# Kernel optimization log

Measured on AMD Instinct MI355X. Metric: run time of the kernel, lower is better.

The kernel has to match this reference:

```python
import jax, jax.numpy as jnp
import numpy as np

N_NODES = 100000
N_EDGES = 1200000
MAX_ATOM_TYPE = 100
NUM_FEATURES = 92
GC_DIM = 64          # pre_layer_dim == gc_dim == CGConv channels
NUM_RBF = 32
NUM_GC_LAYERS = 4
CUTOFF_UPPER = 5.0
BN_EPS = 1e-5


def setup_inputs() -> dict:
    key = jax.random.key(0)
    ks = jax.random.split(key, 12)
    atom_types = jax.random.randint(ks[0], (N_NODES,), 0, MAX_ATOM_TYPE, dtype=jnp.int32)
    pos = jax.random.uniform(ks[1], (N_NODES, 3), dtype=jnp.float32) * 6.0  # box side 6 -> many dists < cutoff
    edge_index = jax.random.randint(ks[2], (2, N_EDGES), 0, N_NODES, dtype=jnp.int32)
    # parameters
    emb = jax.random.normal(ks[3], (MAX_ATOM_TYPE, NUM_FEATURES), dtype=jnp.float32)
    s = 1.0 / np.sqrt(NUM_FEATURES)
    pre_W = jax.random.uniform(ks[4], (NUM_FEATURES, GC_DIM), minval=-s, maxval=s, dtype=jnp.float32)
    pre_b = jnp.zeros((GC_DIM,), jnp.float32)
    zdim = 2 * GC_DIM + NUM_RBF  # [x_i, x_j, edge_attr]
    sz = 1.0 / np.sqrt(zdim)
    Wf = jax.random.uniform(ks[5], (NUM_GC_LAYERS, zdim, GC_DIM), minval=-sz, maxval=sz, dtype=jnp.float32)
    bf = jnp.zeros((NUM_GC_LAYERS, GC_DIM), jnp.float32)
    Ws = jax.random.uniform(ks[6], (NUM_GC_LAYERS, zdim, GC_DIM), minval=-sz, maxval=sz, dtype=jnp.float32)
    bs = jnp.zeros((NUM_GC_LAYERS, GC_DIM), jnp.float32)
    bn_gamma = jnp.ones((NUM_GC_LAYERS, GC_DIM), jnp.float32)
    bn_beta = jnp.zeros((NUM_GC_LAYERS, GC_DIM), jnp.float32)
    # ExpNormalSmearing (torchmd-net) init
    start = np.exp(-CUTOFF_UPPER)
    means = jnp.asarray(np.linspace(start, 1.0, NUM_RBF), jnp.float32)
    betas = jnp.full((NUM_RBF,), (2.0 / NUM_RBF * (1.0 - start)) ** -2, jnp.float32)
    return {"atom_types": atom_types, "pos": pos, "edge_index": edge_index,
            "emb": emb, "pre_W": pre_W, "pre_b": pre_b,
            "Wf": Wf, "bf": bf, "Ws": Ws, "bs": bs,
            "bn_gamma": bn_gamma, "bn_beta": bn_beta,
            "means": means, "betas": betas}


def _forward(atom_types, pos, edge_index, emb, pre_W, pre_b, Wf, bf, Ws, bs,
             bn_gamma, bn_beta, means, betas):
    src, dst = edge_index[0], edge_index[1]
    # distance (edge_vec = pos[src] - pos[dst])
    vec = pos[src] - pos[dst]                                  # [E,3]
    dist = jnp.sqrt(jnp.sum(vec * vec, axis=-1) + 1e-12)       # [E]
    # expnorm RBF with cosine cutoff (cutoff_lower = 0)
    cutoff = 0.5 * (jnp.cos(dist * (np.pi / CUTOFF_UPPER)) + 1.0) * (dist < CUTOFF_UPPER)
    alpha = 5.0 / CUTOFF_UPPER
    edge_attr = cutoff[:, None] * jnp.exp(
        -betas * (jnp.exp(-alpha * dist)[:, None] - means) ** 2)  # [E,NUM_RBF]
    # embedding + pre layer
    x = emb[atom_types]                                        # [N,F]
    x = jax.nn.relu(x @ pre_W + pre_b)                         # [N,C]
    # mean-aggregation degree (scatter-mean denominator)
    deg = jax.ops.segment_sum(jnp.ones_like(dist), dst, num_segments=N_NODES)
    inv_deg = jnp.where(deg > 0, 1.0 / jnp.maximum(deg, 1.0), 0.0)[:, None]
    for l in range(NUM_GC_LAYERS):
        # CGConv: z = [x_i, x_j, e]; out = x + mean_j(sigmoid(lin_f(z)) * softplus(lin_s(z)))
        z = jnp.concatenate([x[dst], x[src], edge_attr], axis=-1)   # [E, 2C+R]
        msg = jax.nn.sigmoid(z @ Wf[l] + bf[l]) * jax.nn.softplus(z @ Ws[l] + bs[l])
        agg = jax.ops.segment_sum(msg, dst, num_segments=N_NODES) * inv_deg
        x = x + agg
        # BatchNorm1d (batch statistics, biased var, as in torch training mode)
        mu = jnp.mean(x, axis=0)
        var = jnp.mean((x - mu) ** 2, axis=0)
        x = (x - mu) * jax.lax.rsqrt(var + BN_EPS) * bn_gamma[l] + bn_beta[l]
    return x


def reference(atom_types, pos, edge_index, emb, pre_W, pre_b, Wf, bf, Ws, bs,
              bn_gamma, bn_beta, means, betas):
    return _forward(atom_types, pos, edge_index, emb, pre_W, pre_b, Wf, bf, Ws, bs,
                    bn_gamma, bn_beta, means, betas)
```

## Files before the change

### kernel.cpp

```cpp
#include <hip/hip_runtime.h>
#include <math.h>

#define N_NODES 100000
#define N_EDGES 1200000
#define GC 64
#define RBF 32
#define NLAYERS 4
#define NF 92
#define NATOM 100
#define BN_EPS 1e-5f
#define TILE_GRID 2048
#define NWIN (N_EDGES / 16)
#define LOG2E 1.44269504f
#define LN2 0.69314718f

typedef _Float16 half8 __attribute__((ext_vector_type(8)));
typedef _Float16 half4 __attribute__((ext_vector_type(4)));
typedef _Float16 half2v __attribute__((ext_vector_type(2)));
typedef float f32x4 __attribute__((ext_vector_type(4)));
union U32H2 { unsigned int u; half2v h; };

__global__ __launch_bounds__(256) void deg_kernel(
    const int* __restrict__ ei, int* __restrict__ deg)
{
    int e = blockIdx.x * 256 + threadIdx.x;
    if (e >= N_EDGES) return;
    atomicAdd(&deg[ei[N_EDGES + e]], 1);
}

__global__ __launch_bounds__(256) void scan_a_kernel(const int* __restrict__ deg, int* __restrict__ bsums)
{
    __shared__ int sm[256];
    int tid = threadIdx.x;
    int i = blockIdx.x * 256 + tid;
    int v = (i < N_NODES) ? deg[i] : 0;
    sm[tid] = v;
    __syncthreads();
    for (int s = 128; s > 0; s >>= 1) {
        if (tid < s) sm[tid] += sm[tid + s];
        __syncthreads();
    }
    if (tid == 0) bsums[blockIdx.x] = sm[0];
}

__global__ __launch_bounds__(512) void scan_b_kernel(const int* __restrict__ bsums, int* __restrict__ boffs)
{
    __shared__ int sm[512];
    int tid = threadIdx.x;
    int v = (tid < 391) ? bsums[tid] : 0;
    sm[tid] = v;
    __syncthreads();
    for (int off = 1; off < 512; off <<= 1) {
        int t = (tid >= off) ? sm[tid - off] : 0;
        __syncthreads();
        sm[tid] += t;
        __syncthreads();
    }
    boffs[tid] = (tid == 0) ? 0 : sm[tid - 1];
}

__global__ __launch_bounds__(256) void scan_c_kernel(
    const int* __restrict__ deg, const int* __restrict__ boffs,
    int* __restrict__ row_st, float* __restrict__ inv_deg)
{
    __shared__ int sm[256];
    int tid = threadIdx.x;
    int i = blockIdx.x * 256 + tid;
    int v = (i < N_NODES) ? deg[i] : 0;
    sm[tid] = v;
    __syncthreads();
    for (int off = 1; off < 256; off <<= 1) {
        int t = (tid >= off) ? sm[tid - off] : 0;
        __syncthreads();
        sm[tid] += t;
        __syncthreads();
    }
    if (i <= N_NODES) row_st[i] = boffs[blockIdx.x] + sm[tid] - v;
    if (i < N_NODES) inv_deg[i] = (v > 0) ? (1.0f / (float)v) : 0.0f;
}

__global__ __launch_bounds__(256) void scatter_perm_kernel(
    const int* __restrict__ ei, const int* __restrict__ row_st,
    int* __restrict__ cursor, int2* __restrict__ csr_sd)
{
    int e = blockIdx.x * 256 + threadIdx.x;
    if (e >= N_EDGES) return;
    int s = ei[e];
    int d = ei[N_EDGES + e];
    int p = atomicAdd(&cursor[d], 1);
    csr_sd[row_st[d] + p] = make_int2(s, d);
}

__global__ __launch_bounds__(256) void split_kernel(
    const int2* __restrict__ csr_sd, int* __restrict__ csr_src, int* __restrict__ csr_dst)
{
    int i = blockIdx.x * 256 + threadIdx.x;
    if (i >= N_EDGES) return;
    int2 v = csr_sd[i];
    csr_src[i] = v.x;
    csr_dst[i] = v.y;
}

__global__ __launch_bounds__(256) void rbf_kernel(
    const int* __restrict__ csr_src, const int* __restrict__ csr_dst,
    const float* __restrict__ pos,
    const float* __restrict__ means, const float* __restrict__ betas,
    unsigned int* __restrict__ ea)
{
    int idx = blockIdx.x * 256 + threadIdx.x;
    if (idx >= N_EDGES) return;
    int s = csr_src[idx];
    int d = csr_dst[idx];
    float dx = pos[s * 3 + 0] - pos[d * 3 + 0];
    float dy = pos[s * 3 + 1] - pos[d * 3 + 1];
    float dz = pos[s * 3 + 2] - pos[d * 3 + 2];
    float dist = sqrtf(dx * dx + dy * dy + dz * dz + 1e-12f);

    float cut = 0.0f;
    if (dist < 5.0f) cut = 0.5f * (__cosf(dist * 0.6283185307179586f) + 1.0f);
    float ex = __expf(-dist);
    union { _Float16 h[32]; uint4 u[4]; } pk;
#pragma unroll
    for (int k = 0; k < 32; k++) {
        float v = ex - means[k];
        pk.h[k] = (_Float16)(cut * __expf(-betas[k] * v * v));
    }
    uint4* op = (uint4*)(ea + (size_t)idx * 16);
    op[0] = pk.u[0];
    op[1] = pk.u[1];
    op[2] = pk.u[2];
    op[3] = pk.u[3];
}

__global__ __launch_bounds__(256) void window_prep_kernel(
    const int* __restrict__ csr_dst, const float* __restrict__ inv_deg,
    unsigned char* __restrict__ seg8, int* __restrict__ wnode, _Float16* __restrict__ inv_e)
{
    int w = blockIdx.x * 256 + threadIdx.x;
    if (w >= NWIN) return;
    int base = w * 16;
    int prev = -1, s = -1;
    for (int k = 0; k < 16; k++) {
        int d = csr_dst[base + k];
        if (d != prev) { s++; prev = d; wnode[base + s] = d; }
        seg8[base + k] = (unsigned char)s;
        inv_e[base + k] = (_Float16)(inv_deg[d] * LN2);
    }
    for (int m = s + 1; m < 16; m++) wnode[base + m] = -1;
}

__global__ __launch_bounds__(256) void wcvt_kernel(
    const float* __restrict__ Wf, const float* __restrict__ Ws,
    _Float16* __restrict__ wf16, _Float16* __restrict__ ws16)
{
    int i = blockIdx.x * 256 + threadIdx.x;
    int l = i / (160 * GC);
    int r = i - l * 160 * GC;
    int k = r >> 6;
    int col = r & 63;
    size_t o = ((size_t)l * GC + col) * 160 + k;
    wf16[o] = (_Float16)(Wf[i] * LOG2E);
    ws16[o] = (_Float16)(Ws[i] * LOG2E);
}

__global__ __launch_bounds__(64) void atom_table_kernel(
    const float* __restrict__ emb, const float* __restrict__ pre_W,
    const float* __restrict__ pre_b, float* __restrict__ T)
{
    int a = blockIdx.x;
    int c = threadIdx.x;
    float acc = pre_b[c];
    for (int k = 0; k < NF; k++) acc = fmaf(emb[a * NF + k], pre_W[k * GC + c], acc);
    T[a * GC + c] = fmaxf(acc, 0.0f);
}

__global__ __launch_bounds__(256) void xinit_kernel(
    const int* __restrict__ atom_types, const float* __restrict__ T,
    float* __restrict__ x, _Float16* __restrict__ x16)
{
    int i = blockIdx.x * 256 + threadIdx.x;
    int n = i >> 4;
    int a = atom_types[n];
    float4 v = ((const float4*)T)[a * 16 + (i & 15)];
    ((float4*)x)[i] = v;
    half4 h = { (_Float16)v.x, (_Float16)v.y, (_Float16)v.z, (_Float16)v.w };
    ((half4*)x16)[i] = h;
}

static __device__ __forceinline__ void proj_mfma16(
    const _Float16* __restrict__ wf, const _Float16* __restrict__ ws,
    const float* __restrict__ bfv, const float* __restrict__ bsv,
    const half8 Bn[2], int cb, int node, unsigned int* __restrict__ P2u)
{
    const int lane = threadIdx.x & 63;
    const int quad = lane >> 4;
    const int r16 = lane & 15;
    f32x4 accf[2], accs[2];
#pragma unroll
    for (int sub = 0; sub < 2; sub++) {
        accf[sub] = (f32x4){0.f, 0.f, 0.f, 0.f};
        accs[sub] = (f32x4){0.f, 0.f, 0.f, 0.f};
    }
#pragma unroll
    for (int kt = 0; kt < 2; kt++) {
#pragma unroll
        for (int sub = 0; sub < 2; sub++) {
            int chan = cb + sub * 16 + r16;
            half8 a = *(const half8*)(wf + (size_t)chan * 160 + kt * 32 + quad * 8);
            half8 b = *(const half8*)(ws + (size_t)chan * 160 + kt * 32 + quad * 8);
            accf[sub] = __builtin_amdgcn_mfma_f32_16x16x32_f16(a, Bn[kt], accf[sub], 0, 0, 0);
            accs[sub] = __builtin_amdgcn_mfma_f32_16x16x32_f16(b, Bn[kt], accs[sub], 0, 0, 0);
        }
    }
#pragma unroll
    for (int sub = 0; sub < 2; sub++) {
        float4 bf4 = *(const float4*)(bfv + cb + sub * 16 + quad * 4);
        float4 bs4 = *(const float4*)(bsv + cb + sub * 16 + quad * 4);
        half8 h = { (_Float16)(accf[sub][0] + bf4.x * LOG2E), (_Float16)(accs[sub][0] + bs4.x * LOG2E),
                    (_Float16)(accf[sub][1] + bf4.y * LOG2E), (_Float16)(accs[sub][1] + bs4.y * LOG2E),
                    (_Float16)(accf[sub][2] + bf4.z * LOG2E), (_Float16)(accs[sub][2] + bs4.z * LOG2E),
                    (_Float16)(accf[sub][3] + bf4.w * LOG2E), (_Float16)(accs[sub][3] + bs4.w * LOG2E) };
        *(half8*)(P2u + (size_t)node * GC + cb + sub * 16 + quad * 4) = h;
    }
}

__global__ __launch_bounds__(256) void proj_kernel(
    const _Float16* __restrict__ x16,
    const _Float16* __restrict__ wf, const _Float16* __restrict__ ws,
    const float* __restrict__ bfv, const float* __restrict__ bsv,
    unsigned int* __restrict__ P2u)
{
    const int lane = threadIdx.x & 63;
    const int wid = threadIdx.x >> 6;
    const int quad = lane >> 4;
    const int r16 = lane & 15;
    const int wgid = blockIdx.x * 4 + wid;
    const int cb = (wgid & 1) * 32;
    const int nb = (wgid >> 1) * 16;
    half8 Bn[2];
    Bn[0] = *(const half8*)(x16 + (size_t)(nb + r16) * GC + quad * 8);
    Bn[1] = *(const half8*)(x16 + (size_t)(nb + r16) * GC + 32 + quad * 8);
    proj_mfma16(wf, ws, bfv, bsv, Bn, cb, nb + r16, P2u);
}

__global__ __launch_bounds__(256) void bnproj_kernel(
    const float* __restrict__ xn, const float* __restrict__ stats,
    const float* __restrict__ gamma, const float* __restrict__ beta,
    float* __restrict__ xout, _Float16* __restrict__ x16,
    const _Float16* __restrict__ wf, const _Float16* __restrict__ ws,
    const float* __restrict__ bfv, const float* __restrict__ bsv,
    unsigned int* __restrict__ P2u)
{
    __shared__ _Float16 lx[32 * 72];
    const int nb = blockIdx.x * 32;
    const float invN = 1.0f / (float)N_NODES;

#pragma unroll
    for (int rep = 0; rep < 2; rep++) {
        int g = rep * 256 + threadIdx.x;
        int gi = blockIdx.x * 512 + g;
        int node = g >> 4;
        int c4 = (g & 15) * 4;
        float4 v = ((const float4*)xn)[gi];
        float vv[4] = {v.x, v.y, v.z, v.w};
        float o[4];
#pragma unroll
        for (int t = 0; t < 4; t++) {
            int c = c4 + t;
            float mu = stats[c] * invN;
            float var = stats[64 + c] * invN - mu * mu;
            float sc = gamma[c] * rsqrtf(var + BN_EPS);
            o[t] = (vv[t] - mu) * sc + beta[c];
        }
        ((float4*)xout)[gi] = make_float4(o[0], o[1], o[2], o[3]);
        half4 h = { (_Float16)o[0], (_Float16)o[1], (_Float16)o[2], (_Float16)o[3] };
        ((half4*)x16)[gi] = h;
        *(half4*)(lx + node * 72 + c4) = h;
    }
    __syncthreads();

    const int lane = threadIdx.x & 63;
    const int wid = threadIdx.x >> 6;
    const int quad = lane >> 4;
    const int r16 = lane & 15;
    const int cb = (wid & 1) * 32;
    const int tn = (wid >> 1) * 16 + r16;
    half8 Bn[2];
    Bn[0] = *(const half8*)(lx + tn * 72 + quad * 8);
    Bn[1] = *(const half8*)(lx + tn * 72 + 32 + quad * 8);
    proj_mfma16(wf, ws, bfv, bsv, Bn, cb, nb + tn, P2u);
}

static __device__ __forceinline__ void compute_win(
    half8 S0, half8 S1, half8 E, int4 d4, int moff,
    const half8 (&WGF)[3][2], const half8 (&WGS)[3][2],
    int r16, int quad, int cb,
    const unsigned char* __restrict__ seg8, const int* __restrict__ wnode,
    const _Float16* __restrict__ inv_e, const unsigned int* __restrict__ P2u,
    float* __restrict__ x)
{
    unsigned int pv0, pv1, pv2, pv3, pv4, pv5, pv6, pv7;
    {
        const unsigned int* p0 = P2u + (size_t)d4.x * GC + cb + r16;
        const unsigned int* p1 = P2u + (size_t)d4.y * GC + cb + r16;
        const unsigned int* p2 = P2u + (size_t)d4.z * GC + cb + r16;
        const unsigned int* p3 = P2u + (size_t)d4.w * GC + cb + r16;
        pv0 = p0[0];  pv4 = p0[16];
        pv1 = p1[0];  pv5 = p1[16];
        pv2 = p2[0];  pv6 = p2[16];
        pv3 = p3[0];  pv7 = p3[16];
    }
    unsigned int segq = *(const unsigned int*)(seg8 + moff + quad * 4);
    int4 wn4 = *(const int4*)(wnode + moff + quad * 4);
    half4 inv4 = *(const half4*)(inv_e + moff + quad * 4);

    const f32x4 zf = (f32x4){0.0f, 0.0f, 0.0f, 0.0f};
    f32x4 accf[2], accs[2];
    __builtin_amdgcn_s_setprio(1);
#pragma unroll
    for (int ctl = 0; ctl < 2; ctl++) {
        accf[ctl] = __builtin_amdgcn_mfma_f32_16x16x32_f16(S0, WGF[0][ctl], zf, 0, 0, 0);
        accs[ctl] = __builtin_amdgcn_mfma_f32_16x16x32_f16(S0, WGS[0][ctl], zf, 0, 0, 0);
        accf[ctl] = __builtin_amdgcn_mfma_f32_16x16x32_f16(S1, WGF[1][ctl], accf[ctl], 0, 0, 0);
        accs[ctl] = __builtin_amdgcn_mfma_f32_16x16x32_f16(S1, WGS[1][ctl], accs[ctl], 0, 0, 0);
        accf[ctl] = __builtin_amdgcn_mfma_f32_16x16x32_f16(E,  WGF[2][ctl], accf[ctl], 0, 0, 0);
        accs[ctl] = __builtin_amdgcn_mfma_f32_16x16x32_f16(E,  WGS[2][ctl], accs[ctl], 0, 0, 0);
    }
    __builtin_amdgcn_s_setprio(0);

    unsigned int pvv[8] = {pv0, pv1, pv2, pv3, pv4, pv5, pv6, pv7};
    half4 msgh[2];
#pragma unroll
    for (int ctl = 0; ctl < 2; ctl++) {
#pragma unroll
        for (int rr = 0; rr < 4; rr++) {
            U32H2 t; t.u = pvv[ctl * 4 + rr];
            float af = accf[ctl][rr] + (float)t.h.x;
            float as = accs[ctl][rr] + (float)t.h.y;
            float sg = __builtin_amdgcn_rcpf(1.0f + __builtin_amdgcn_exp2f(-af));
            float sp = __builtin_amdgcn_logf(1.0f + __builtin_amdgcn_exp2f(as));
            msgh[ctl][rr] = (_Float16)(sg * sp);
        }
    }
    half4 am;
#pragma unroll
    for (int j = 0; j < 4; j++) {
        int sj = (segq >> (8 * j)) & 0xff;
        am[j] = (sj == r16) ? inv4[j] : (_Float16)0.0f;
    }
    int wa[4] = { wn4.x, wn4.y, wn4.z, wn4.w };
#pragma unroll
    for (int ctl = 0; ctl < 2; ctl++) {
        f32x4 red = __builtin_amdgcn_mfma_f32_16x16x16f16(am, msgh[ctl], zf, 0, 0, 0);
#pragma unroll
        for (int rr = 0; rr < 4; rr++) {
            int nd = wa[rr];
            if (nd >= 0) atomicAdd(&x[(size_t)nd * GC + cb + ctl * 16 + r16], red[rr]);
        }
    }
}

#define LOADSET(S0_, S1_, EE_, SRC_, WW_)                                            \
    S0_ = *(const half8*)(x16 + (size_t)(SRC_) * GC + quad * 8);                     \
    S1_ = *(const half8*)(x16 + (size_t)(SRC_) * GC + 32 + quad * 8);                \
    EE_ = *(const half8*)(ea + ((size_t)(WW_) * 16 + r16) * RBF + quad * 8);

__global__ __launch_bounds__(256, 4) void win_mfma_kernel(
    const _Float16* __restrict__ x16, const _Float16* __restrict__ ea,
    const int* __restrict__ csr_src, const int* __restrict__ csr_dst,
    const unsigned char* __restrict__ seg8, const int* __restrict__ wnode,
    const _Float16* __restrict__ inv_e, const unsigned int* __restrict__ P2u,
    const _Float16* __restrict__ wf16, const _Float16* __restrict__ ws16,
    float* __restrict__ x)
{
    const int lane = threadIdx.x & 63;
    const int wid = __builtin_amdgcn_readfirstlane(threadIdx.x >> 6);
    const int quad = lane >> 4;
    const int r16 = lane & 15;
    const int wgid = blockIdx.x * 4 + wid;
    const int cb = (wgid & 1) * 32;
    int w = wgid >> 1;
    const int NSEQ = TILE_GRID * 2;

    half8 WGF[3][2], WGS[3][2];
#pragma unroll
    for (int ctl = 0; ctl < 2; ctl++) {
        const _Float16* wfp = wf16 + (size_t)(cb + ctl * 16 + r16) * 160 + 64 + quad * 8;
        const _Float16* wsp = ws16 + (size_t)(cb + ctl * 16 + r16) * 160 + 64 + quad * 8;
#pragma unroll
        for (int kt = 0; kt < 3; kt++) {
            WGF[kt][ctl] = *(const half8*)(wfp + kt * 32);
            WGS[kt][ctl] = *(const half8*)(wsp + kt * 32);
        }
    }

    int sA = csr_src[w * 16 + r16];
    int4 d4A = *(const int4*)(csr_dst + w * 16 + quad * 4);
    half8 AS0, AS1, AE;
    LOADSET(AS0, AS1, AE, sA, w);
    int moffA = w * 16;

    int wB = w + NSEQ; if (wB >= NWIN) wB = NWIN - 1;
    int sB = csr_src[wB * 16 + r16];
    int4 d4B = *(const int4*)(csr_dst + wB * 16 + quad * 4);
    half8 BS0, BS1, BE;
    LOADSET(BS0, BS1, BE, sB, wB);
    int moffB = wB * 16;

    int wC = wB + NSEQ; if (wC >= NWIN) wC = NWIN - 1;
    int sC = csr_src[wC * 16 + r16];
    int4 d4C = *(const int4*)(csr_dst + wC * 16 + quad * 4);

    while (true) {
        compute_win(AS0, AS1, AE, d4A, moffA,
                    WGF, WGS, r16, quad, cb, seg8, wnode, inv_e, P2u, x);
        LOADSET(AS0, AS1, AE, sC, wC);
        d4A = d4C; moffA = wC * 16;
        wC += NSEQ; if (wC >= NWIN) wC = NWIN - 1;
        sC = csr_src[wC * 16 + r16];
        d4C = *(const int4*)(csr_dst + wC * 16 + quad * 4);
        w += NSEQ;
        if (w >= NWIN) break;

        compute_win(BS0, BS1, BE, d4B, moffB,
                    WGF, WGS, r16, quad, cb, seg8, wnode, inv_e, P2u, x);
        LOADSET(BS0, BS1, BE, sC, wC);
        d4B = d4C; moffB = wC * 16;
        wC += NSEQ; if (wC >= NWIN) wC = NWIN - 1;
        sC = csr_src[wC * 16 + r16];
        d4C = *(const int4*)(csr_dst + wC * 16 + quad * 4);
        w += NSEQ;
        if (w >= NWIN) break;
    }
}

__global__ __launch_bounds__(256) void stats_kernel(const float* __restrict__ x, float* __restrict__ stats)
{
    const int lane = threadIdx.x & 63;
    const int wid = threadIdx.x >> 6;
    int w = blockIdx.x * 4 + wid;
    float s1 = 0.0f, s2 = 0.0f;
    for (int n = w; n < N_NODES; n += 1024) {
        float v = x[(size_t)n * GC + lane];
        s1 += v;
        s2 = fmaf(v, v, s2);
    }
    __shared__ float rs1[4][64];
    __shared__ float rs2[4][64];
    rs1[wid][lane] = s1;
    rs2[wid][lane] = s2;
    __syncthreads();
    if (threadIdx.x < 64) {
        atomicAdd(&stats[lane], rs1[0][lane] + rs1[1][lane] + rs1[2][lane] + rs1[3][lane]);
    } else if (threadIdx.x < 128) {
        int c = threadIdx.x & 63;
        atomicAdd(&stats[64 + c], rs2[0][c] + rs2[1][c] + rs2[2][c] + rs2[3][c]);
    }
}

__global__ __launch_bounds__(256) void bn_kernel(
    const float* __restrict__ xn, const float* __restrict__ stats,
    const float* __restrict__ gamma, const float* __restrict__ beta,
    float* __restrict__ out)
{
    int i = blockIdx.x * 256 + threadIdx.x;
    int c4 = (i & 15) * 4;
    float4 v = ((const float4*)xn)[i];
    float vv[4] = {v.x, v.y, v.z, v.w};
    float o[4];
    const float invN = 1.0f / (float)N_NODES;
#pragma unroll
    for (int t = 0; t < 4; t++) {
        int c = c4 + t;
        float mu = stats[c] * invN;
        float var = stats[64 + c] * invN - mu * mu;
        float sc = gamma[c] * rsqrtf(var + BN_EPS);
        o[t] = (vv[t] - mu) * sc + beta[c];
    }
    ((float4*)out)[i] = make_float4(o[0], o[1], o[2], o[3]);
}

extern "C" void kernel_launch(void* const* d_in, const int* in_sizes, int n_in,
                              void* d_out, int out_size, void* d_ws, size_t ws_size,
                              hipStream_t stream)
{
    const int* atom_types = (const int*)d_in[0];
    const float* pos = (const float*)d_in[1];
    const int* edge_index = (const int*)d_in[2];
    const float* emb = (const float*)d_in[3];
    const float* pre_W = (const float*)d_in[4];
    const float* pre_b = (const float*)d_in[5];
    const float* Wf = (const float*)d_in[6];
    const float* bf = (const float*)d_in[7];
    const float* Ws = (const float*)d_in[8];
    const float* bs = (const float*)d_in[9];
    const float* gamma = (const float*)d_in[10];
    const float* beta = (const float*)d_in[11];
    const float* means = (const float*)d_in[12];
    const float* betas = (const float*)d_in[13];

    char* base = (char*)d_ws;
    char* p = base;
    auto alloc = [&](size_t bytes) -> char* {
        char* r = p;
        p += (bytes + 255) & ~(size_t)255;
        return r;
    };
    unsigned int* ea = (unsigned int*)alloc((size_t)N_EDGES * RBF * 2);
    float* x = (float*)alloc((size_t)N_NODES * GC * 4);
    _Float16* x16 = (_Float16*)alloc((size_t)N_NODES * GC * 2);
    unsigned int* P2u = (unsigned int*)alloc((size_t)N_NODES * GC * 4);
    int* csr_src = (int*)alloc((size_t)N_EDGES * 4);
    int* csr_dst = (int*)alloc((size_t)N_EDGES * 4);
    int* wnode = (int*)alloc((size_t)N_EDGES * 4);
    unsigned char* seg8 = (unsigned char*)alloc((size_t)N_EDGES);
    _Float16* inv_e = (_Float16*)alloc((size_t)N_EDGES * 2);
    _Float16* wf16 = (_Float16*)alloc((size_t)NLAYERS * GC * 160 * 2);
    _Float16* ws16 = (_Float16*)alloc((size_t)NLAYERS * GC * 160 * 2);
    int* row_st = (int*)alloc((size_t)(N_NODES + 1) * 4);
    float* inv_deg = (float*)alloc((size_t)N_NODES * 4);
    float* T = (float*)alloc((size_t)NATOM * GC * 4);
    int* bsums = (int*)alloc(512 * 4);
    int* boffs = (int*)alloc(512 * 4);
    const size_t ZR_INTS = (size_t)2 * N_NODES + 128 * NLAYERS + 64;
    char* zr = alloc(ZR_INTS * 4);
    int* deg = (int*)zr;
    int* cursor = deg + N_NODES;
    float* stats = (float*)(cursor + N_NODES);

    int2* csr_sd = (int2*)ea;

    if ((size_t)(p - base) > ws_size) return;

    (void)hipMemsetAsync(zr, 0, ZR_INTS * 4, stream);

    const int EG = (N_EDGES + 255) / 256;
    deg_kernel<<<EG, 256, 0, stream>>>(edge_index, deg);
    scan_a_kernel<<<391, 256, 0, stream>>>(deg, bsums);
    scan_b_kernel<<<1, 512, 0, stream>>>(bsums, boffs);
    scan_c_kernel<<<391, 256, 0, stream>>>(deg, boffs, row_st, inv_deg);
    scatter_perm_kernel<<<EG, 256, 0, stream>>>(edge_index, row_st, cursor, csr_sd);
    split_kernel<<<EG, 256, 0, stream>>>(csr_sd, csr_src, csr_dst);
    rbf_kernel<<<EG, 256, 0, stream>>>(csr_src, csr_dst, pos, means, betas, ea);
    window_prep_kernel<<<(NWIN + 255) / 256, 256, 0, stream>>>(csr_dst, inv_deg, seg8, wnode, inv_e);
    wcvt_kernel<<<(NLAYERS * 160 * GC) / 256, 256, 0, stream>>>(Wf, Ws, wf16, ws16);
    atom_table_kernel<<<NATOM, 64, 0, stream>>>(emb, pre_W, pre_b, T);
    xinit_kernel<<<N_NODES * 16 / 256, 256, 0, stream>>>(atom_types, T, x, x16);
    proj_kernel<<<N_NODES / 32, 256, 0, stream>>>(x16, wf16, ws16, bf, bs, P2u);

    for (int l = 0; l < NLAYERS; l++) {
        win_mfma_kernel<<<TILE_GRID, 256, 0, stream>>>(
            x16, (const _Float16*)ea, csr_src, csr_dst, seg8, wnode, inv_e, P2u,
            wf16 + (size_t)l * GC * 160, ws16 + (size_t)l * GC * 160, x);
        stats_kernel<<<256, 256, 0, stream>>>(x, stats + l * 128);
        if (l < NLAYERS - 1) {
            bnproj_kernel<<<N_NODES / 32, 256, 0, stream>>>(
                x, stats + l * 128, gamma + l * GC, beta + l * GC, x, x16,
                wf16 + (size_t)(l + 1) * GC * 160, ws16 + (size_t)(l + 1) * GC * 160,
                bf + (l + 1) * GC, bs + (l + 1) * GC, P2u);
        } else {
            bn_kernel<<<N_NODES * 16 / 256, 256, 0, stream>>>(
                x, stats + l * 128, gamma + l * GC, beta + l * GC, (float*)d_out);
        }
    }
}
```

Baseline: 891.2 us.

## Process all 64 channels per wave with LDS-staged weight fragments

Each wave now handles a full 16-edge window across all 64 output channels instead of splitting channels between two waves. This halves the redundant gathers of source features, edge attributes and window metadata. Weight fragments are pre-swizzled into an MFMA-friendly layout by the conversion kernel and staged in shared memory per block, rather than held in registers. The grid drops to 768 blocks with an occupancy hint of 3. In exchange each MFMA step reads its weights from LDS, accumulator register pressure doubles, and fewer waves are resident.

```diff
diff --git a/kernel.cpp b/kernel.cpp
--- a/kernel.cpp
+++ b/kernel.cpp
@@ -9,7 +9,7 @@
 #define NF 92
 #define NATOM 100
 #define BN_EPS 1e-5f
-#define TILE_GRID 2048
+#define WIN_GRID 768
 #define NWIN (N_EDGES / 16)
 #define LOG2E 1.44269504f
 #define LN2 0.69314718f
@@ -151,16 +151,27 @@
 
 __global__ __launch_bounds__(256) void wcvt_kernel(
     const float* __restrict__ Wf, const float* __restrict__ Ws,
-    _Float16* __restrict__ wf16, _Float16* __restrict__ ws16)
+    _Float16* __restrict__ wf16, _Float16* __restrict__ ws16,
+    _Float16* __restrict__ wfrag)
 {
     int i = blockIdx.x * 256 + threadIdx.x;
     int l = i / (160 * GC);
     int r = i - l * 160 * GC;
     int k = r >> 6;
     int col = r & 63;
+    _Float16 vf = (_Float16)(Wf[i] * LOG2E);
+    _Float16 vs = (_Float16)(Ws[i] * LOG2E);
     size_t o = ((size_t)l * GC + col) * 160 + k;
-    wf16[o] = (_Float16)(Wf[i] * LOG2E);
-    ws16[o] = (_Float16)(Ws[i] * LOG2E);
+    wf16[o] = vf;
+    ws16[o] = vs;
+    if (k >= 64) {
+        int kk = k - 64;
+        int f = kk >> 3;
+        int j = kk & 7;
+        size_t ob = ((size_t)l * 2 * 12 + f) * 512 + col * 8 + j;
+        wfrag[ob] = vf;
+        wfrag[ob + 12 * 512] = vs;
+    }
 }
 
 __global__ __launch_bounds__(64) void atom_table_kernel(
@@ -293,48 +304,57 @@
 
 static __device__ __forceinline__ void compute_win(
     half8 S0, half8 S1, half8 E, int4 d4, int moff,
-    const half8 (&WGF)[3][2], const half8 (&WGS)[3][2],
-    int r16, int quad, int cb,
+    const _Float16* __restrict__ wl,
+    int r16, int quad,
     const unsigned char* __restrict__ seg8, const int* __restrict__ wnode,
     const _Float16* __restrict__ inv_e, const unsigned int* __restrict__ P2u,
     float* __restrict__ x)
 {
-    unsigned int pv0, pv1, pv2, pv3, pv4, pv5, pv6, pv7;
+    unsigned int pv[4][4];
     {
-        const unsigned int* p0 = P2u + (size_t)d4.x * GC + cb + r16;
-        const unsigned int* p1 = P2u + (size_t)d4.y * GC + cb + r16;
-        const unsigned int* p2 = P2u + (size_t)d4.z * GC + cb + r16;
-        const unsigned int* p3 = P2u + (size_t)d4.w * GC + cb + r16;
-        pv0 = p0[0];  pv4 = p0[16];
-        pv1 = p1[0];  pv5 = p1[16];
-        pv2 = p2[0];  pv6 = p2[16];
-        pv3 = p3[0];  pv7 = p3[16];
+        const unsigned int* pb0 = P2u + (size_t)d4.x * GC + r16;
+        const unsigned int* pb1 = P2u + (size_t)d4.y * GC + r16;
+        const unsigned int* pb2 = P2u + (size_t)d4.z * GC + r16;
+        const unsigned int* pb3 = P2u + (size_t)d4.w * GC + r16;
+#pragma unroll
+        for (int ctl = 0; ctl < 4; ctl++) {
+            pv[ctl][0] = pb0[ctl * 16];
+            pv[ctl][1] = pb1[ctl * 16];
+            pv[ctl][2] = pb2[ctl * 16];
+            pv[ctl][3] = pb3[ctl * 16];
+        }
     }
     unsigned int segq = *(const unsigned int*)(seg8 + moff + quad * 4);
     int4 wn4 = *(const int4*)(wnode + moff + quad * 4);
     half4 inv4 = *(const half4*)(inv_e + moff + quad * 4);
 
     const f32x4 zf = (f32x4){0.0f, 0.0f, 0.0f, 0.0f};
-    f32x4 accf[2], accs[2];
+    f32x4 accf[4], accs[4];
     __builtin_amdgcn_s_setprio(1);
 #pragma unroll
-    for (int ctl = 0; ctl < 2; ctl++) {
-        accf[ctl] = __builtin_amdgcn_mfma_f32_16x16x32_f16(S0, WGF[0][ctl], zf, 0, 0, 0);
-        accs[ctl] = __builtin_amdgcn_mfma_f32_16x16x32_f16(S0, WGS[0][ctl], zf, 0, 0, 0);
-        accf[ctl] = __builtin_amdgcn_mfma_f32_16x16x32_f16(S1, WGF[1][ctl], accf[ctl], 0, 0, 0);
-        accs[ctl] = __builtin_amdgcn_mfma_f32_16x16x32_f16(S1, WGS[1][ctl], accs[ctl], 0, 0, 0);
-        accf[ctl] = __builtin_amdgcn_mfma_f32_16x16x32_f16(E,  WGF[2][ctl], accf[ctl], 0, 0, 0);
-        accs[ctl] = __builtin_amdgcn_mfma_f32_16x16x32_f16(E,  WGS[2][ctl], accs[ctl], 0, 0, 0);
+    for (int ctl = 0; ctl < 4; ctl++) {
+        const int co = quad * 512 + (ctl * 16 + r16) * 8;
+        half8 wf0 = *(const half8*)(wl + co);
+        half8 ws0 = *(const half8*)(wl + 12 * 512 + co);
+        half8 wf1 = *(const half8*)(wl + 4 * 512 + co);
+        half8 ws1 = *(const half8*)(wl + 16 * 512 + co);
+        half8 wf2 = *(const half8*)(wl + 8 * 512 + co);
+        half8 ws2 = *(const half8*)(wl + 20 * 512 + co);
+        accf[ctl] = __builtin_amdgcn_mfma_f32_16x16x32_f16(S0, wf0, zf, 0, 0, 0);
+        accs[ctl] = __builtin_amdgcn_mfma_f32_16x16x32_f16(S0, ws0, zf, 0, 0, 0);
+        accf[ctl] = __builtin_amdgcn_mfma_f32_16x16x32_f16(S1, wf1, accf[ctl], 0, 0, 0);
+        accs[ctl] = __builtin_amdgcn_mfma_f32_16x16x32_f16(S1, ws1, accs[ctl], 0, 0, 0);
+        accf[ctl] = __builtin_amdgcn_mfma_f32_16x16x32_f16(E,  wf2, accf[ctl], 0, 0, 0);
+        accs[ctl] = __builtin_amdgcn_mfma_f32_16x16x32_f16(E,  ws2, accs[ctl], 0, 0, 0);
     }
     __builtin_amdgcn_s_setprio(0);
 
-    unsigned int pvv[8] = {pv0, pv1, pv2, pv3, pv4, pv5, pv6, pv7};
-    half4 msgh[2];
-#pragma unroll
-    for (int ctl = 0; ctl < 2; ctl++) {
+    half4 msgh[4];
+#pragma unroll
+    for (int ctl = 0; ctl < 4; ctl++) {
 #pragma unroll
         for (int rr = 0; rr < 4; rr++) {
-            U32H2 t; t.u = pvv[ctl * 4 + rr];
+            U32H2 t; t.u = pv[ctl][rr];
             float af = accf[ctl][rr] + (float)t.h.x;
             float as = accs[ctl][rr] + (float)t.h.y;
             float sg = __builtin_amdgcn_rcpf(1.0f + __builtin_amdgcn_exp2f(-af));
@@ -350,12 +370,12 @@
     }
     int wa[4] = { wn4.x, wn4.y, wn4.z, wn4.w };
 #pragma unroll
-    for (int ctl = 0; ctl < 2; ctl++) {
+    for (int ctl = 0; ctl < 4; ctl++) {
         f32x4 red = __builtin_amdgcn_mfma_f32_16x16x16f16(am, msgh[ctl], zf, 0, 0, 0);
 #pragma unroll
         for (int rr = 0; rr < 4; rr++) {
             int nd = wa[rr];
-            if (nd >= 0) atomicAdd(&x[(size_t)nd * GC + cb + ctl * 16 + r16], red[rr]);
+            if (nd >= 0) atomicAdd(&x[(size_t)nd * GC + ctl * 16 + r16], red[rr]);
         }
     }
 }
@@ -365,34 +385,26 @@
     S1_ = *(const half8*)(x16 + (size_t)(SRC_) * GC + 32 + quad * 8);                \
     EE_ = *(const half8*)(ea + ((size_t)(WW_) * 16 + r16) * RBF + quad * 8);
 
-__global__ __launch_bounds__(256, 4) void win_mfma_kernel(
+__global__ __launch_bounds__(256, 3) void win_mfma_kernel(
     const _Float16* __restrict__ x16, const _Float16* __restrict__ ea,
     const int* __restrict__ csr_src, const int* __restrict__ csr_dst,
     const unsigned char* __restrict__ seg8, const int* __restrict__ wnode,
     const _Float16* __restrict__ inv_e, const unsigned int* __restrict__ P2u,
-    const _Float16* __restrict__ wf16, const _Float16* __restrict__ ws16,
+    const _Float16* __restrict__ wfl,
     float* __restrict__ x)
 {
+    __shared__ __align__(16) _Float16 wl[2 * 12 * 512];
+#pragma unroll
+    for (int i = threadIdx.x; i < 1536; i += 256)
+        ((half8*)wl)[i] = ((const half8*)wfl)[i];
+    __syncthreads();
+
     const int lane = threadIdx.x & 63;
     const int wid = __builtin_amdgcn_readfirstlane(threadIdx.x >> 6);
     const int quad = lane >> 4;
     const int r16 = lane & 15;
-    const int wgid = blockIdx.x * 4 + wid;
-    const int cb = (wgid & 1) * 32;
-    int w = wgid >> 1;
-    const int NSEQ = TILE_GRID * 2;
-
-    half8 WGF[3][2], WGS[3][2];
-#pragma unroll
-    for (int ctl = 0; ctl < 2; ctl++) {
-        const _Float16* wfp = wf16 + (size_t)(cb + ctl * 16 + r16) * 160 + 64 + quad * 8;
-        const _Float16* wsp = ws16 + (size_t)(cb + ctl * 16 + r16) * 160 + 64 + quad * 8;
-#pragma unroll
-        for (int kt = 0; kt < 3; kt++) {
-            WGF[kt][ctl] = *(const half8*)(wfp + kt * 32);
-            WGS[kt][ctl] = *(const half8*)(wsp + kt * 32);
-        }
-    }
+    int w = blockIdx.x * 4 + wid;
+    const int NSEQ = WIN_GRID * 4;
 
     int sA = csr_src[w * 16 + r16];
     int4 d4A = *(const int4*)(csr_dst + w * 16 + quad * 4);
@@ -413,7 +425,7 @@
 
     while (true) {
         compute_win(AS0, AS1, AE, d4A, moffA,
-                    WGF, WGS, r16, quad, cb, seg8, wnode, inv_e, P2u, x);
+                    wl, r16, quad, seg8, wnode, inv_e, P2u, x);
         LOADSET(AS0, AS1, AE, sC, wC);
         d4A = d4C; moffA = wC * 16;
         wC += NSEQ; if (wC >= NWIN) wC = NWIN - 1;
@@ -423,7 +435,7 @@
         if (w >= NWIN) break;
 
         compute_win(BS0, BS1, BE, d4B, moffB,
-                    WGF, WGS, r16, quad, cb, seg8, wnode, inv_e, P2u, x);
+                    wl, r16, quad, seg8, wnode, inv_e, P2u, x);
         LOADSET(BS0, BS1, BE, sC, wC);
         d4B = d4C; moffB = wC * 16;
         wC += NSEQ; if (wC >= NWIN) wC = NWIN - 1;
@@ -517,6 +529,7 @@
     _Float16* inv_e = (_Float16*)alloc((size_t)N_EDGES * 2);
     _Float16* wf16 = (_Float16*)alloc((size_t)NLAYERS * GC * 160 * 2);
     _Float16* ws16 = (_Float16*)alloc((size_t)NLAYERS * GC * 160 * 2);
+    _Float16* wfrag = (_Float16*)alloc((size_t)NLAYERS * 2 * 12 * 512 * 2);
     int* row_st = (int*)alloc((size_t)(N_NODES + 1) * 4);
     float* inv_deg = (float*)alloc((size_t)N_NODES * 4);
     float* T = (float*)alloc((size_t)NATOM * GC * 4);
@@ -543,15 +556,15 @@
     split_kernel<<<EG, 256, 0, stream>>>(csr_sd, csr_src, csr_dst);
     rbf_kernel<<<EG, 256, 0, stream>>>(csr_src, csr_dst, pos, means, betas, ea);
     window_prep_kernel<<<(NWIN + 255) / 256, 256, 0, stream>>>(csr_dst, inv_deg, seg8, wnode, inv_e);
-    wcvt_kernel<<<(NLAYERS * 160 * GC) / 256, 256, 0, stream>>>(Wf, Ws, wf16, ws16);
+    wcvt_kernel<<<(NLAYERS * 160 * GC) / 256, 256, 0, stream>>>(Wf, Ws, wf16, ws16, wfrag);
     atom_table_kernel<<<NATOM, 64, 0, stream>>>(emb, pre_W, pre_b, T);
     xinit_kernel<<<N_NODES * 16 / 256, 256, 0, stream>>>(atom_types, T, x, x16);
     proj_kernel<<<N_NODES / 32, 256, 0, stream>>>(x16, wf16, ws16, bf, bs, P2u);
 
     for (int l = 0; l < NLAYERS; l++) {
-        win_mfma_kernel<<<TILE_GRID, 256, 0, stream>>>(
+        win_mfma_kernel<<<WIN_GRID, 256, 0, stream>>>(
             x16, (const _Float16*)ea, csr_src, csr_dst, seg8, wnode, inv_e, P2u,
-            wf16 + (size_t)l * GC * 160, ws16 + (size_t)l * GC * 160, x);
+            wfrag + (size_t)l * 2 * 12 * 512, x);
         stats_kernel<<<256, 256, 0, stream>>>(x, stats + l * 128);
         if (l < NLAYERS - 1) {
             bnproj_kernel<<<N_NODES / 32, 256, 0, stream>>>(
```

Result: slower. 952.0 us (+6.8%).
